# Kernel optimization log

Measured on AMD Instinct MI355X. Metric: run time of the kernel, lower is better.

The kernel has to match this reference:

```python
import jax, jax.numpy as jnp
import numpy as np

N, E, H, R = 20000, 400000, 128, 20


def setup_inputs() -> dict:
    key = jax.random.key(0)
    ks = jax.random.split(key, 12)
    inv_h = 1.0 / np.sqrt(H)
    inv_r = 1.0 / np.sqrt(R)
    return {
        "s": jax.random.normal(ks[0], (N, H), jnp.float32),
        "v": jax.random.normal(ks[1], (N, 3, H), jnp.float32),
        "edge_rbf": jax.random.normal(ks[2], (E, R), jnp.float32),
        "edge_cutoff": jax.random.uniform(ks[3], (E,), jnp.float32),
        "edge_vec": jax.random.normal(ks[4], (E, 3), jnp.float32),
        "W1": jax.random.normal(ks[5], (H, H), jnp.float32) * inv_h,
        "b1": jnp.zeros((H,), jnp.float32),
        "W2": jax.random.normal(ks[6], (H, 3 * H), jnp.float32) * inv_h,
        "b2": jnp.zeros((3 * H,), jnp.float32),
        "Wr": jax.random.normal(ks[7], (R, 3 * H), jnp.float32) * inv_r,
        "br": jnp.zeros((3 * H,), jnp.float32),
        "edge_index": jax.random.randint(ks[8], (2, E), 0, N, jnp.int64),
    }


def reference(s, v, edge_rbf, edge_cutoff, edge_vec, W1, b1, W2, b2, Wr, br, edge_index):
    i, j = edge_index[0], edge_index[1]
    n = s.shape[0]
    # rbf projection modulated by cutoff: [E, 3H]
    W = (edge_rbf @ Wr + br) * edge_cutoff[:, None]
    # scalar MLP on gathered source features: [E, 3H]
    h = jax.nn.silu(s[j] @ W1 + b1)
    x = (h @ W2 + b2) * W
    x_ss, x_sv, x_vv = jnp.split(x, 3, axis=-1)  # each [E, H]
    ds = jax.ops.segment_sum(x_ss, i, num_segments=n)
    # dv1: outer product of edge direction with gated scalars -> [E,3,H]
    dv1 = jax.ops.segment_sum(x_sv[:, None, :] * edge_vec[:, :, None], i, num_segments=n)
    # equivariant term: project v_j onto edge direction, re-expand
    inner = jnp.sum(v[j] * edge_vec[:, :, None], axis=1)  # [E, H]
    dv2 = jax.ops.segment_sum((inner * x_vv)[:, None, :] * edge_vec[:, :, None], i, num_segments=n)
    return ds, dv1 + dv2
```

## Files before the change

### kernel.cpp

```cpp
#include <hip/hip_runtime.h>

#define HDIM 128
#define H3   384
#define RDIM 20
#define NPB  8
#define CHNK 64

__global__ __launch_bounds__(128) void node_mlp_kernel(
    const float* __restrict__ s, const float* __restrict__ W1,
    const float* __restrict__ b1, const float* __restrict__ W2,
    const float* __restrict__ b2, float* __restrict__ P, int N)
{
    __shared__ float sS[NPB][HDIM];
    __shared__ float sH[NPB][HDIM];
    const int t  = threadIdx.x;
    const int n0 = blockIdx.x * NPB;

    #pragma unroll
    for (int n = 0; n < NPB; ++n) {
        int node = n0 + n;
        sS[n][t] = (node < N) ? s[(size_t)node * HDIM + t] : 0.f;
    }
    __syncthreads();

    float acc[NPB];
    #pragma unroll
    for (int n = 0; n < NPB; ++n) acc[n] = 0.f;
    for (int k = 0; k < HDIM; ++k) {
        float w = W1[k * HDIM + t];
        #pragma unroll
        for (int n = 0; n < NPB; ++n) acc[n] += sS[n][k] * w;
    }
    float bb = b1[t];
    #pragma unroll
    for (int n = 0; n < NPB; ++n) {
        float z = acc[n] + bb;
        sH[n][t] = z / (1.f + __expf(-z));
    }
    __syncthreads();

    float a0[NPB], a1[NPB], a2[NPB];
    #pragma unroll
    for (int n = 0; n < NPB; ++n) { a0[n] = 0.f; a1[n] = 0.f; a2[n] = 0.f; }
    for (int k = 0; k < HDIM; ++k) {
        float w0 = W2[k * H3 + t];
        float w1 = W2[k * H3 + t + 128];
        float w2 = W2[k * H3 + t + 256];
        #pragma unroll
        for (int n = 0; n < NPB; ++n) {
            float hv = sH[n][k];
            a0[n] += hv * w0;
            a1[n] += hv * w1;
            a2[n] += hv * w2;
        }
    }
    float c0 = b2[t], c1 = b2[t + 128], c2 = b2[t + 256];
    #pragma unroll
    for (int n = 0; n < NPB; ++n) {
        int node = n0 + n;
        if (node < N) {
            size_t base = (size_t)node * H3;
            P[base + t]       = a0[n] + c0;
            P[base + t + 128] = a1[n] + c1;
            P[base + t + 256] = a2[n] + c2;
        }
    }
}

__global__ void hist_kernel(const int* __restrict__ eidx, int* __restrict__ counts, int E)
{
    int e = blockIdx.x * 256 + threadIdx.x;
    if (e < E) atomicAdd(&counts[eidx[e]], 1);
}

__global__ __launch_bounds__(1024) void scan_kernel(
    const int* __restrict__ counts, int* __restrict__ rstart,
    int* __restrict__ cursor, int N)
{
    __shared__ int part[1024];
    const int t = threadIdx.x;
    const int C = 20;
    int loc[C];
    int s = 0;
    #pragma unroll
    for (int q = 0; q < C; ++q) {
        int idx = t * C + q;
        int c = (idx < N) ? counts[idx] : 0;
        loc[q] = s; s += c;
    }
    part[t] = s;
    __syncthreads();
    for (int off = 1; off < 1024; off <<= 1) {
        int vv = (t >= off) ? part[t - off] : 0;
        __syncthreads();
        part[t] += vv;
        __syncthreads();
    }
    int boff = (t > 0) ? part[t - 1] : 0;
    #pragma unroll
    for (int q = 0; q < C; ++q) {
        int idx = t * C + q;
        if (idx < N) {
            int st = boff + loc[q];
            rstart[idx] = st;
            cursor[idx] = st;
        }
    }
    if (t == 1023) rstart[N] = part[1023];
}

__global__ void scatter_kernel(const int* __restrict__ eidx, int* __restrict__ cursor,
                               int* __restrict__ eord, int E)
{
    int e = blockIdx.x * 256 + threadIdx.x;
    if (e < E) {
        int i = eidx[e];
        int pos = atomicAdd(&cursor[i], 1);
        eord[pos] = e;
    }
}

__global__ __launch_bounds__(128) void reduce_kernel(
    const int* __restrict__ rstart, const int* __restrict__ eord,
    const float* __restrict__ rbf, const float* __restrict__ cutoff,
    const float* __restrict__ evec, const float* __restrict__ Wr,
    const float* __restrict__ br, const float* __restrict__ P,
    const float* __restrict__ v, const int* __restrict__ eidx,
    float* __restrict__ ds, float* __restrict__ dv, int E)
{
    const int t = threadIdx.x;
    const int i = blockIdx.x;

    float wr0[RDIM], wr1[RDIM], wr2[RDIM];
    #pragma unroll
    for (int k = 0; k < RDIM; ++k) {
        wr0[k] = Wr[k * H3 + t];
        wr1[k] = Wr[k * H3 + t + 128];
        wr2[k] = Wr[k * H3 + t + 256];
    }
    float br0 = br[t], br1 = br[t + 128], br2 = br[t + 256];

    int beg = rstart[i], end = rstart[i + 1];
    float accs = 0.f, accx = 0.f, accy = 0.f, accz = 0.f;

    __shared__ int sE[CHNK], sJ[CHNK];

    for (int c0 = beg; c0 < end; c0 += CHNK) {
        int cnt = min(CHNK, end - c0);
        __syncthreads();
        if (t < cnt) {
            int e = eord[c0 + t];
            sE[t] = e;
            sJ[t] = eidx[E + e];
        }
        __syncthreads();
        for (int q = 0; q < cnt; ++q) {
            int e = sE[q], j = sJ[q];
            float cu = cutoff[e];
            float ex = evec[3 * e], ey = evec[3 * e + 1], ez = evec[3 * e + 2];
            const float4* rb4 = (const float4*)(rbf + (size_t)e * RDIM);
            float w0 = 0.f, w1 = 0.f, w2 = 0.f;
            #pragma unroll
            for (int k4 = 0; k4 < 5; ++k4) {
                float4 r = rb4[k4];
                w0 += r.x * wr0[4*k4+0] + r.y * wr0[4*k4+1] + r.z * wr0[4*k4+2] + r.w * wr0[4*k4+3];
                w1 += r.x * wr1[4*k4+0] + r.y * wr1[4*k4+1] + r.z * wr1[4*k4+2] + r.w * wr1[4*k4+3];
                w2 += r.x * wr2[4*k4+0] + r.y * wr2[4*k4+1] + r.z * wr2[4*k4+2] + r.w * wr2[4*k4+3];
            }
            size_t pj = (size_t)j * H3;
            float xss = (w0 + br0) * cu * P[pj + t];
            float xsv = (w1 + br1) * cu * P[pj + 128 + t];
            float xvv = (w2 + br2) * cu * P[pj + 256 + t];
            float inner = v[pj + t] * ex + v[pj + 128 + t] * ey + v[pj + 256 + t] * ez;
            float coef = xsv + inner * xvv;
            accs += xss;
            accx += coef * ex;
            accy += coef * ey;
            accz += coef * ez;
        }
    }

    size_t di  = (size_t)i * HDIM;
    size_t dvi = (size_t)i * H3;
    ds[di + t]        = accs;
    dv[dvi + t]       = accx;
    dv[dvi + 128 + t] = accy;
    dv[dvi + 256 + t] = accz;
}

extern "C" void kernel_launch(void* const* d_in, const int* in_sizes, int n_in,
                              void* d_out, int out_size, void* d_ws, size_t ws_size,
                              hipStream_t stream)
{
    const float* s    = (const float*)d_in[0];
    const float* v    = (const float*)d_in[1];
    const float* rbf  = (const float*)d_in[2];
    const float* cut  = (const float*)d_in[3];
    const float* evec = (const float*)d_in[4];
    const float* W1   = (const float*)d_in[5];
    const float* b1   = (const float*)d_in[6];
    const float* W2   = (const float*)d_in[7];
    const float* b2   = (const float*)d_in[8];
    const float* Wr   = (const float*)d_in[9];
    const float* br   = (const float*)d_in[10];
    const int*   eidx = (const int*)d_in[11];

    const int N = in_sizes[0] / HDIM;
    const int E = in_sizes[3];

    float* out = (float*)d_out;
    float* ds  = out;
    float* dv  = out + (size_t)N * HDIM;

    char* w = (char*)d_ws;
    float* P      = (float*)w;                       w += (size_t)N * H3 * sizeof(float);
    int*   counts = (int*)w;                         w += ((size_t)N * 4 + 255) / 256 * 256;
    int*   rstart = (int*)w;                         w += ((size_t)(N + 1) * 4 + 255) / 256 * 256;
    int*   cursor = (int*)w;                         w += ((size_t)N * 4 + 255) / 256 * 256;
    int*   eord   = (int*)w;

    hipMemsetAsync(counts, 0, (size_t)N * sizeof(int), stream);

    node_mlp_kernel<<<(N + NPB - 1) / NPB, 128, 0, stream>>>(s, W1, b1, W2, b2, P, N);
    hist_kernel<<<(E + 255) / 256, 256, 0, stream>>>(eidx, counts, E);
    scan_kernel<<<1, 1024, 0, stream>>>(counts, rstart, cursor, N);
    scatter_kernel<<<(E + 255) / 256, 256, 0, stream>>>(eidx, cursor, eord, E);
    reduce_kernel<<<N, 128, 0, stream>>>(rstart, eord, rbf, cut, evec, Wr, br, P, v,
                                         eidx, ds, dv, E);
}
```

Before: 319.5 us.

## Store gathered node features in bf16 and stage edge data in shared memory

The node MLP output P and a converted copy of v are stored as bf16, which halves the bytes gathered per edge in the reduce kernel. Per-edge cutoff, edge vector and rbf values are loaded cooperatively into shared memory once per chunk rather than being read redundantly by every thread. The next edge's gathered values are prefetched into registers during the current edge's work. It also doubles the nodes per block in the MLP, halves the chunk size, and adds a v conversion kernel, trading precision for bandwidth.

```diff
diff --git a/kernel.cpp b/kernel.cpp
--- a/kernel.cpp
+++ b/kernel.cpp
@@ -1,15 +1,28 @@
 #include <hip/hip_runtime.h>
+#include <hip/hip_bf16.h>
 
 #define HDIM 128
 #define H3   384
 #define RDIM 20
-#define NPB  8
-#define CHNK 64
+#define NPB  16
+#define CHNK 32
+
+typedef unsigned short u16;
+
+__device__ __forceinline__ float bf2f(u16 u) {
+    union { unsigned int i; float f; } x;
+    x.i = ((unsigned int)u) << 16;
+    return x.f;
+}
+__device__ __forceinline__ u16 f2bf(float f) {
+    __hip_bfloat16 h = __float2bfloat16(f);
+    return *(u16*)&h;
+}
 
 __global__ __launch_bounds__(128) void node_mlp_kernel(
     const float* __restrict__ s, const float* __restrict__ W1,
     const float* __restrict__ b1, const float* __restrict__ W2,
-    const float* __restrict__ b2, float* __restrict__ P, int N)
+    const float* __restrict__ b2, u16* __restrict__ P, int N)
 {
     __shared__ float sS[NPB][HDIM];
     __shared__ float sH[NPB][HDIM];
@@ -42,16 +55,23 @@
     float a0[NPB], a1[NPB], a2[NPB];
     #pragma unroll
     for (int n = 0; n < NPB; ++n) { a0[n] = 0.f; a1[n] = 0.f; a2[n] = 0.f; }
-    for (int k = 0; k < HDIM; ++k) {
-        float w0 = W2[k * H3 + t];
-        float w1 = W2[k * H3 + t + 128];
-        float w2 = W2[k * H3 + t + 256];
+    for (int k2 = 0; k2 < HDIM / 2; ++k2) {
+        float2 hv[NPB];
         #pragma unroll
-        for (int n = 0; n < NPB; ++n) {
-            float hv = sH[n][k];
-            a0[n] += hv * w0;
-            a1[n] += hv * w1;
-            a2[n] += hv * w2;
+        for (int n = 0; n < NPB; ++n) hv[n] = ((const float2*)sH[n])[k2];
+        #pragma unroll
+        for (int kk = 0; kk < 2; ++kk) {
+            int k = 2 * k2 + kk;
+            float w0 = W2[k * H3 + t];
+            float w1 = W2[k * H3 + t + 128];
+            float w2 = W2[k * H3 + t + 256];
+            #pragma unroll
+            for (int n = 0; n < NPB; ++n) {
+                float h = kk ? hv[n].y : hv[n].x;
+                a0[n] += h * w0;
+                a1[n] += h * w1;
+                a2[n] += h * w2;
+            }
         }
     }
     float c0 = b2[t], c1 = b2[t + 128], c2 = b2[t + 256];
@@ -60,10 +80,22 @@
         int node = n0 + n;
         if (node < N) {
             size_t base = (size_t)node * H3;
-            P[base + t]       = a0[n] + c0;
-            P[base + t + 128] = a1[n] + c1;
-            P[base + t + 256] = a2[n] + c2;
-        }
+            P[base + t]       = f2bf(a0[n] + c0);
+            P[base + t + 128] = f2bf(a1[n] + c1);
+            P[base + t + 256] = f2bf(a2[n] + c2);
+        }
+    }
+}
+
+__global__ void vconv_kernel(const float* __restrict__ v, u16* __restrict__ Vb, int nquads)
+{
+    int idx = blockIdx.x * 256 + threadIdx.x;
+    int stride = gridDim.x * 256;
+    for (; idx < nquads; idx += stride) {
+        float4 f = ((const float4*)v)[idx];
+        ushort4 o;
+        o.x = f2bf(f.x); o.y = f2bf(f.y); o.z = f2bf(f.z); o.w = f2bf(f.w);
+        ((ushort4*)Vb)[idx] = o;
     }
 }
 
@@ -124,8 +156,8 @@
     const int* __restrict__ rstart, const int* __restrict__ eord,
     const float* __restrict__ rbf, const float* __restrict__ cutoff,
     const float* __restrict__ evec, const float* __restrict__ Wr,
-    const float* __restrict__ br, const float* __restrict__ P,
-    const float* __restrict__ v, const int* __restrict__ eidx,
+    const float* __restrict__ br, const u16* __restrict__ Pb,
+    const u16* __restrict__ Vb, const int* __restrict__ eidx,
     float* __restrict__ ds, float* __restrict__ dv, int E)
 {
     const int t = threadIdx.x;
@@ -143,46 +175,69 @@
     int beg = rstart[i], end = rstart[i + 1];
     float accs = 0.f, accx = 0.f, accy = 0.f, accz = 0.f;
 
-    __shared__ int sE[CHNK], sJ[CHNK];
+    __shared__ int   sE[CHNK], sJ[CHNK];
+    __shared__ float sCut[CHNK], sVx[CHNK], sVy[CHNK], sVz[CHNK];
+    __shared__ __attribute__((aligned(16))) float sRbf[CHNK][RDIM];
 
     for (int c0 = beg; c0 < end; c0 += CHNK) {
         int cnt = min(CHNK, end - c0);
         __syncthreads();
         if (t < cnt) {
             int e = eord[c0 + t];
-            sE[t] = e;
-            sJ[t] = eidx[E + e];
-        }
-        __syncthreads();
+            sE[t]   = e;
+            sJ[t]   = eidx[E + e];
+            sCut[t] = cutoff[e];
+            sVx[t]  = evec[3 * e];
+            sVy[t]  = evec[3 * e + 1];
+            sVz[t]  = evec[3 * e + 2];
+        }
+        __syncthreads();
+        for (int x = t; x < cnt * RDIM; x += 128) {
+            int n = x / RDIM, k = x - n * RDIM;
+            sRbf[n][k] = rbf[(size_t)sE[n] * RDIM + k];
+        }
+        __syncthreads();
+
+        u16 cpss, cpsv, cpvv, cvx, cvy, cvz;
+        {
+            size_t pj = (size_t)sJ[0] * H3;
+            cpss = Pb[pj + t]; cpsv = Pb[pj + 128 + t]; cpvv = Pb[pj + 256 + t];
+            cvx  = Vb[pj + t]; cvy  = Vb[pj + 128 + t]; cvz  = Vb[pj + 256 + t];
+        }
         for (int q = 0; q < cnt; ++q) {
-            int e = sE[q], j = sJ[q];
-            float cu = cutoff[e];
-            float ex = evec[3 * e], ey = evec[3 * e + 1], ez = evec[3 * e + 2];
-            const float4* rb4 = (const float4*)(rbf + (size_t)e * RDIM);
+            u16 npss = 0, npsv = 0, npvv = 0, nvx = 0, nvy = 0, nvz = 0;
+            if (q + 1 < cnt) {
+                size_t pj = (size_t)sJ[q + 1] * H3;
+                npss = Pb[pj + t]; npsv = Pb[pj + 128 + t]; npvv = Pb[pj + 256 + t];
+                nvx  = Vb[pj + t]; nvy  = Vb[pj + 128 + t]; nvz  = Vb[pj + 256 + t];
+            }
+            const float4* r4 = (const float4*)sRbf[q];
             float w0 = 0.f, w1 = 0.f, w2 = 0.f;
             #pragma unroll
             for (int k4 = 0; k4 < 5; ++k4) {
-                float4 r = rb4[k4];
+                float4 r = r4[k4];
                 w0 += r.x * wr0[4*k4+0] + r.y * wr0[4*k4+1] + r.z * wr0[4*k4+2] + r.w * wr0[4*k4+3];
                 w1 += r.x * wr1[4*k4+0] + r.y * wr1[4*k4+1] + r.z * wr1[4*k4+2] + r.w * wr1[4*k4+3];
                 w2 += r.x * wr2[4*k4+0] + r.y * wr2[4*k4+1] + r.z * wr2[4*k4+2] + r.w * wr2[4*k4+3];
             }
-            size_t pj = (size_t)j * H3;
-            float xss = (w0 + br0) * cu * P[pj + t];
-            float xsv = (w1 + br1) * cu * P[pj + 128 + t];
-            float xvv = (w2 + br2) * cu * P[pj + 256 + t];
-            float inner = v[pj + t] * ex + v[pj + 128 + t] * ey + v[pj + 256 + t] * ez;
-            float coef = xsv + inner * xvv;
+            float cu = sCut[q];
+            float ex = sVx[q], ey = sVy[q], ez = sVz[q];
+            float xss = (w0 + br0) * cu * bf2f(cpss);
+            float xsv = (w1 + br1) * cu * bf2f(cpsv);
+            float xvv = (w2 + br2) * cu * bf2f(cpvv);
+            float inner = bf2f(cvx) * ex + bf2f(cvy) * ey + bf2f(cvz) * ez;
+            float coef  = xsv + inner * xvv;
             accs += xss;
             accx += coef * ex;
             accy += coef * ey;
             accz += coef * ez;
-        }
-    }
-
-    size_t di  = (size_t)i * HDIM;
+            cpss = npss; cpsv = npsv; cpvv = npvv;
+            cvx = nvx; cvy = nvy; cvz = nvz;
+        }
+    }
+
+    ds[(size_t)i * HDIM + t] = accs;
     size_t dvi = (size_t)i * H3;
-    ds[di + t]        = accs;
     dv[dvi + t]       = accx;
     dv[dvi + 128 + t] = accy;
     dv[dvi + 256 + t] = accz;
@@ -213,18 +268,20 @@
     float* dv  = out + (size_t)N * HDIM;
 
     char* w = (char*)d_ws;
-    float* P      = (float*)w;                       w += (size_t)N * H3 * sizeof(float);
-    int*   counts = (int*)w;                         w += ((size_t)N * 4 + 255) / 256 * 256;
-    int*   rstart = (int*)w;                         w += ((size_t)(N + 1) * 4 + 255) / 256 * 256;
-    int*   cursor = (int*)w;                         w += ((size_t)N * 4 + 255) / 256 * 256;
-    int*   eord   = (int*)w;
+    u16* P  = (u16*)w;                     w += ((size_t)N * H3 * 2 + 255) / 256 * 256;
+    u16* Vb = (u16*)w;                     w += ((size_t)N * H3 * 2 + 255) / 256 * 256;
+    int* counts = (int*)w;                 w += ((size_t)N * 4 + 255) / 256 * 256;
+    int* rstart = (int*)w;                 w += ((size_t)(N + 1) * 4 + 255) / 256 * 256;
+    int* cursor = (int*)w;                 w += ((size_t)N * 4 + 255) / 256 * 256;
+    int* eord   = (int*)w;
 
     hipMemsetAsync(counts, 0, (size_t)N * sizeof(int), stream);
 
+    vconv_kernel<<<1024, 256, 0, stream>>>(v, Vb, N * H3 / 4);
     node_mlp_kernel<<<(N + NPB - 1) / NPB, 128, 0, stream>>>(s, W1, b1, W2, b2, P, N);
     hist_kernel<<<(E + 255) / 256, 256, 0, stream>>>(eidx, counts, E);
     scan_kernel<<<1, 1024, 0, stream>>>(counts, rstart, cursor, N);
     scatter_kernel<<<(E + 255) / 256, 256, 0, stream>>>(eidx, cursor, eord, E);
-    reduce_kernel<<<N, 128, 0, stream>>>(rstart, eord, rbf, cut, evec, Wr, br, P, v,
+    reduce_kernel<<<N, 128, 0, stream>>>(rstart, eord, rbf, cut, evec, Wr, br, P, Vb,
                                          eidx, ds, dv, E);
 }
```

Measured after the change: 338.4 us. 1.06x slower.
